# Performance work log

Hardware: AMD Instinct MI355X
Metric: run time of the kernel (lower is better)

Reference implementation:

```python
import jax, jax.numpy as jnp
import numpy as np

N, E, G = 20000, 480000, 200
HID = 32  # hidden_channels


def setup_inputs() -> dict:
    key = jax.random.key(0)
    ks = jax.random.split(key, 40)
    rn = lambda k, shape, s=0.1: jax.random.normal(k, shape, jnp.float32) * s
    inp = {
        "x": jax.random.normal(ks[0], (N, 8), jnp.float32),
        "edge_index": jax.random.randint(ks[1], (2, E), 0, N),
        "edge_attr": jax.random.normal(ks[2], (E, 4), jnp.float32),
        "batch": jnp.sort(jax.random.randint(ks[3], (N,), 0, G)),
        "descriptors": jax.random.normal(ks[4], (G, 48), jnp.float32),
        # edge encoder Linear(4 -> 32)
        "We_enc": rn(ks[5], (4, HID)), "be_enc": rn(ks[6], (HID,)),
        # gat1: GATConv(8 -> 32, heads=4, concat)
        "W1": rn(ks[7], (8, 4 * HID)), "as1": rn(ks[8], (4, HID)), "ad1": rn(ks[9], (4, HID)), "b1": rn(ks[10], (4 * HID,)),
        # gat2: GATConv(128 -> 32, heads=4, concat, edge_dim=32)
        "W2": rn(ks[11], (4 * HID, 4 * HID)), "We2": rn(ks[12], (HID, 4 * HID)),
        "as2": rn(ks[13], (4, HID)), "ad2": rn(ks[14], (4, HID)), "ae2": rn(ks[15], (4, HID)), "b2": rn(ks[16], (4 * HID,)),
        # gat3
        "W3": rn(ks[17], (4 * HID, 4 * HID)), "We3": rn(ks[18], (HID, 4 * HID)),
        "as3": rn(ks[19], (4, HID)), "ad3": rn(ks[20], (4, HID)), "ae3": rn(ks[21], (4, HID)), "b3": rn(ks[22], (4 * HID,)),
        # gat4: heads=1, concat=False
        "W4": rn(ks[23], (4 * HID, HID)), "We4": rn(ks[24], (HID, HID)),
        "as4": rn(ks[25], (1, HID)), "ad4": rn(ks[26], (1, HID)), "ae4": rn(ks[27], (1, HID)), "b4": rn(ks[28], (HID,)),
        # descriptor net Linear(48 -> 32)
        "Wd": rn(ks[29], (48, HID)), "bd": rn(ks[30], (HID,)),
        # final Linear(64 -> 1)
        "Wl": rn(ks[31], (2 * HID, 1)), "bl": rn(ks[32], (1,)),
    }
    return inp


def _gat(x, src, dst, n, W, att_s, att_d, bias, heads, ch, concat, e=None, We=None, att_e=None):
    """PyG GATConv: add self-loops (edge fill='mean'), edge softmax over incoming edges."""
    loops = jnp.arange(n)
    if e is not None:
        cnt = jnp.zeros((n,), x.dtype).at[dst].add(1.0)
        loop_e = jnp.zeros((n, e.shape[1]), x.dtype).at[dst].add(e) / jnp.maximum(cnt, 1.0)[:, None]
        e = jnp.concatenate([e, loop_e], axis=0)  # [E+N, edge_dim]
    s = jnp.concatenate([src, loops])
    d = jnp.concatenate([dst, loops])
    h = (x @ W).reshape(n, heads, ch)                      # [N,H,C]
    a_s = (h * att_s).sum(-1)                              # [N,H]
    a_d = (h * att_d).sum(-1)
    alpha = a_s[s] + a_d[d]                                # [E+N,H]
    if e is not None:
        eh = (e @ We).reshape(-1, heads, ch)
        alpha = alpha + (eh * att_e).sum(-1)
    alpha = jax.nn.leaky_relu(alpha, 0.2)
    amax = jax.ops.segment_max(alpha, d, num_segments=n)
    ex = jnp.exp(alpha - amax[d])
    den = jax.ops.segment_sum(ex, d, num_segments=n)
    alpha = ex / (den[d] + 1e-16)
    out = jax.ops.segment_sum(alpha[:, :, None] * h[s], d, num_segments=n)  # [N,H,C]
    out = out.reshape(n, heads * ch) if concat else out.mean(axis=1)
    return out + bias


def reference(x, edge_index, edge_attr, batch, descriptors,
              We_enc, be_enc,
              W1, as1, ad1, b1,
              W2, We2, as2, ad2, ae2, b2,
              W3, We3, as3, ad3, ae3, b3,
              W4, We4, as4, ad4, ae4, b4,
              Wd, bd, Wl, bl):
    src, dst = edge_index[0], edge_index[1]
    n = x.shape[0]
    edge_emb = edge_attr @ We_enc + be_enc                # [E,32]
    h = jax.nn.relu(_gat(x, src, dst, n, W1, as1, ad1, b1, 4, HID, True))
    h = jax.nn.relu(_gat(h, src, dst, n, W2, as2, ad2, b2, 4, HID, True, edge_emb, We2, ae2))
    h = jax.nn.relu(_gat(h, src, dst, n, W3, as3, ad3, b3, 4, HID, True, edge_emb, We3, ae3))
    h = _gat(h, src, dst, n, W4, as4, ad4, b4, 1, HID, False, edge_emb, We4, ae4)  # [N,32]
    # global mean pool per graph
    g_sum = jax.ops.segment_sum(h, batch, num_segments=G)
    g_cnt = jax.ops.segment_sum(jnp.ones((n,), h.dtype), batch, num_segments=G)
    graph_emb = g_sum / jnp.maximum(g_cnt, 1.0)[:, None]  # [G,32]
    desc_emb = jax.nn.relu(descriptors @ Wd + bd)          # [G,32]
    combined = jnp.concatenate([graph_emb, desc_emb], axis=1)
    return jax.nn.sigmoid(combined @ Wl + bl).reshape(-1)  # [G]
```

## Files before the change

kernel.cpp:

```cpp
#include <hip/hip_runtime.h>
#include <hip/hip_bf16.h>
#include <math.h>

#define NN 20000
#define EE 480000
#define GG 200
#define CAP 96

typedef unsigned int uint32;

static __device__ inline unsigned short f2bf(float f) {
  __hip_bfloat16 h = __float2bfloat16(f);
  return *reinterpret_cast<const unsigned short*>(&h);
}
static __device__ inline float bf2f(unsigned short u) {
  return __uint_as_float(((uint32)u) << 16);
}
static __device__ inline float bf_lo(uint32 u) { return __uint_as_float(u << 16); }
static __device__ inline float bf_hi(uint32 u) { return __uint_as_float(u & 0xffff0000u); }
static __device__ inline uint32 pack2(float lo, float hi) {
  return ((uint32)f2bf(lo)) | (((uint32)f2bf(hi)) << 16);
}

__global__ void hist_kernel(const int* __restrict__ dst, int* __restrict__ cnt) {
  int i = blockIdx.x * 256 + threadIdx.x;
  if (i < EE) atomicAdd(&cnt[dst[i]], 1);
}

__global__ void scan1_kernel(const int* __restrict__ cnt, int* __restrict__ row_ptr,
                             int* __restrict__ partial) {
  __shared__ int buf[1024];
  int t = threadIdx.x;
  int i = blockIdx.x * 1024 + t;
  int v = (i < NN) ? cnt[i] : 0;
  buf[t] = v;
  __syncthreads();
  for (int offd = 1; offd < 1024; offd <<= 1) {
    int tmp = (t >= offd) ? buf[t - offd] : 0;
    __syncthreads();
    buf[t] += tmp;
    __syncthreads();
  }
  if (i < NN) row_ptr[i + 1] = buf[t];
  if (t == 1023) partial[blockIdx.x] = buf[1023];
}

__global__ void scan2_kernel(int* __restrict__ partial, int nblk) {
  int t = threadIdx.x;
  int v = (t < nblk) ? partial[t] : 0;
  for (int offd = 1; offd < 32; offd <<= 1) {
    int u = __shfl_up(v, offd);
    if (t >= offd) v += u;
  }
  if (t < nblk) partial[t] = v;
}

__global__ void scan3_kernel(int* __restrict__ row_ptr, const int* __restrict__ partial) {
  int i = blockIdx.x * 256 + threadIdx.x;
  if (i == 0) row_ptr[0] = 0;
  if (i >= 1 && i <= NN) {
    int b = (i - 1) >> 10;
    if (b > 0) row_ptr[i] += partial[b - 1];
  }
}

__global__ void scatter_kernel(const int* __restrict__ src, const int* __restrict__ dst,
                               const float* __restrict__ attr, const int* __restrict__ row_ptr,
                               int* __restrict__ pos, int* __restrict__ csr_src,
                               uint2* __restrict__ attr_pk) {
  int e = blockIdx.x * 256 + threadIdx.x;
  if (e >= EE) return;
  int d = dst[e];
  int p = row_ptr[d] + atomicAdd(&pos[d], 1);
  csr_src[p] = src[e];
  float4 a = ((const float4*)attr)[e];
  uint2 q;
  q.x = pack2(a.x, a.y);
  q.y = pack2(a.z, a.w);
  attr_pk[p] = q;
}

#define AMB ((NN + 255) / 256)

__global__ void aux_kernel(const int* __restrict__ row_ptr, const uint2* __restrict__ attr_pk,
                           float* __restrict__ mean_attr, const int* __restrict__ batch,
                           int* __restrict__ bound, const float* __restrict__ We_enc,
                           const float* __restrict__ be_enc, const float* __restrict__ We2,
                           const float* __restrict__ ae2, const float* __restrict__ We3,
                           const float* __restrict__ ae3, const float* __restrict__ We4,
                           const float* __restrict__ ae4, float* __restrict__ fold) {
  int b = blockIdx.x;
  int t = threadIdx.x;
  if (b < AMB) {
    int node = b * 256 + t;
    if (node < NN) {
      int p0 = row_ptr[node], p1 = row_ptr[node + 1];
      float s0 = 0.f, s1 = 0.f, s2 = 0.f, s3 = 0.f;
      for (int p = p0; p < p1; ++p) {
        uint2 q = attr_pk[p];
        s0 += bf_lo(q.x); s1 += bf_hi(q.x);
        s2 += bf_lo(q.y); s3 += bf_hi(q.y);
      }
      int deg = p1 - p0;
      float inv = 1.f / (float)(deg > 1 ? deg : 1);
      ((float4*)mean_attr)[node] = make_float4(s0 * inv, s1 * inv, s2 * inv, s3 * inv);
    }
    return;
  }
  if (b < 2 * AMB) {
    int i = (b - AMB) * 256 + t;
    if (i >= NN) return;
    int bc = batch[i];
    int bp = (i == 0) ? -1 : batch[i - 1];
    for (int g = bp + 1; g <= bc; ++g) bound[g] = i;
    if (i == NN - 1)
      for (int g = bc + 1; g <= GG; ++g) bound[g] = NN;
    return;
  }
  __shared__ float V[32 * 4];
  if (t < 128) {
    int k = t >> 2, h = t & 3;
    float s = 0.f;
    for (int c = 0; c < 32; ++c) s = fmaf(We2[k * 128 + h * 32 + c], ae2[h * 32 + c], s);
    V[k * 4 + h] = s;
  }
  __syncthreads();
  if (t < 16) {
    int i = t >> 2, h = t & 3;
    float s = 0.f;
    for (int k = 0; k < 32; ++k) s = fmaf(We_enc[i * 32 + k], V[k * 4 + h], s);
    fold[i * 4 + h] = s;
  } else if (t < 20) {
    int h = t - 16;
    float s = 0.f;
    for (int k = 0; k < 32; ++k) s = fmaf(be_enc[k], V[k * 4 + h], s);
    fold[16 + h] = s;
  }
  __syncthreads();
  if (t < 128) {
    int k = t >> 2, h = t & 3;
    float s = 0.f;
    for (int c = 0; c < 32; ++c) s = fmaf(We3[k * 128 + h * 32 + c], ae3[h * 32 + c], s);
    V[k * 4 + h] = s;
  }
  __syncthreads();
  if (t < 16) {
    int i = t >> 2, h = t & 3;
    float s = 0.f;
    for (int k = 0; k < 32; ++k) s = fmaf(We_enc[i * 32 + k], V[k * 4 + h], s);
    fold[20 + i * 4 + h] = s;
  } else if (t < 20) {
    int h = t - 16;
    float s = 0.f;
    for (int k = 0; k < 32; ++k) s = fmaf(be_enc[k], V[k * 4 + h], s);
    fold[36 + h] = s;
  }
  __syncthreads();
  if (t < 32) {
    float s = 0.f;
    for (int c = 0; c < 32; ++c) s = fmaf(We4[t * 32 + c], ae4[c], s);
    V[t] = s;
  }
  __syncthreads();
  if (t < 4) {
    float s = 0.f;
    for (int k = 0; k < 32; ++k) s = fmaf(We_enc[t * 32 + k], V[k], s);
    fold[40 + t] = s;
  } else if (t == 4) {
    float s = 0.f;
    for (int k = 0; k < 32; ++k) s = fmaf(be_enc[k], V[k], s);
    fold[44] = s;
  }
}

__global__ void gemm1_kernel(const float* __restrict__ X, const float* __restrict__ W,
                             const float* __restrict__ att_s, const float* __restrict__ att_d,
                             __hip_bfloat16* __restrict__ H, float* __restrict__ a_s,
                             float* __restrict__ a_d) {
  constexpr int K = 8;
  constexpr int COLS = 128;
  constexpr int ROWS = 8;
  __shared__ float xs[ROWS][K];
  int tid = threadIdx.x;
  int row0 = blockIdx.x * ROWS;
  if (tid < ROWS * K) xs[tid / K][tid % K] = X[row0 * K + tid];
  __syncthreads();
  int c = tid;
  float acc[ROWS];
#pragma unroll
  for (int j = 0; j < ROWS; ++j) acc[j] = 0.f;
  for (int k = 0; k < K; ++k) {
    float wv = W[k * COLS + c];
#pragma unroll
    for (int j = 0; j < ROWS; ++j) acc[j] = fmaf(xs[j][k], wv, acc[j]);
  }
  float asv = att_s[c], adv = att_d[c];
#pragma unroll
  for (int j = 0; j < ROWS; ++j) {
    int row = row0 + j;
    float vs = acc[j] * asv, vd = acc[j] * adv;
#pragma unroll
    for (int m = 16; m >= 1; m >>= 1) {
      vs += __shfl_xor(vs, m);
      vd += __shfl_xor(vd, m);
    }
    H[row * COLS + c] = __float2bfloat16(acc[j]);
    if ((tid & 31) == 0) {
      a_s[row * 4 + (c >> 5)] = vs;
      a_d[row * 4 + (c >> 5)] = vd;
    }
  }
}

template <int COLS, int TR>
__global__ __launch_bounds__(256) void gemm2_kernel(const float* __restrict__ X,
                                                    const float* __restrict__ W,
                                                    const float* __restrict__ att_s,
                                                    const float* __restrict__ att_d,
                                                    __hip_bfloat16* __restrict__ H,
                                                    float* __restrict__ a_s,
                                                    float* __restrict__ a_d) {
  constexpr int K = 128;
  constexpr int HEADS = COLS / 32;
  constexpr int CG = COLS / 4;
  constexpr int RG = 256 / CG;
  constexpr int ROWS = RG * TR;
  __shared__ unsigned short ws[K * COLS];
  __shared__ float xs[ROWS * K];
  int tid = threadIdx.x;
  int row0 = blockIdx.x * ROWS;
  for (int i = tid * 4; i < K * COLS; i += 1024) {
    float4 wv = *(const float4*)&W[i];
    ushort4 u;
    u.x = f2bf(wv.x); u.y = f2bf(wv.y); u.z = f2bf(wv.z); u.w = f2bf(wv.w);
    *(ushort4*)&ws[i] = u;
  }
  for (int i = tid * 4; i < ROWS * K; i += 1024) {
    int grow = row0 + i / K;
    float4 v = make_float4(0.f, 0.f, 0.f, 0.f);
    if (grow < NN) v = *(const float4*)&X[(size_t)grow * K + (i & (K - 1))];
    *(float4*)&xs[i] = v;
  }
  __syncthreads();
  int cg = tid % CG, rg = tid / CG;
  int c0 = cg * 4, r0 = rg * TR;
  float acc[TR][4];
#pragma unroll
  for (int i = 0; i < TR; ++i)
#pragma unroll
    for (int j = 0; j < 4; ++j) acc[i][j] = 0.f;
  for (int k0 = 0; k0 < K; k0 += 4) {
    float w4[4][4];
#pragma unroll
    for (int j = 0; j < 4; ++j) {
      ushort4 u = *(ushort4*)&ws[(k0 + j) * COLS + c0];
      w4[j][0] = bf2f(u.x); w4[j][1] = bf2f(u.y); w4[j][2] = bf2f(u.z); w4[j][3] = bf2f(u.w);
    }
#pragma unroll
    for (int i = 0; i < TR; ++i) {
      float4 xv = *(float4*)&xs[(r0 + i) * K + k0];
#pragma unroll
      for (int j = 0; j < 4; ++j) {
        acc[i][j] = fmaf(xv.x, w4[0][j], acc[i][j]);
        acc[i][j] = fmaf(xv.y, w4[1][j], acc[i][j]);
        acc[i][j] = fmaf(xv.z, w4[2][j], acc[i][j]);
        acc[i][j] = fmaf(xv.w, w4[3][j], acc[i][j]);
      }
    }
  }
  float as4[4], ad4[4];
#pragma unroll
  for (int j = 0; j < 4; ++j) { as4[j] = att_s[c0 + j]; ad4[j] = att_d[c0 + j]; }
  int h = c0 >> 5;
#pragma unroll
  for (int i = 0; i < TR; ++i) {
    int row = row0 + r0 + i;
    ushort4 hv;
    hv.x = f2bf(acc[i][0]); hv.y = f2bf(acc[i][1]); hv.z = f2bf(acc[i][2]); hv.w = f2bf(acc[i][3]);
    if (row < NN) *(ushort4*)&H[(size_t)row * COLS + c0] = hv;
    float vs = 0.f, vd = 0.f;
#pragma unroll
    for (int j = 0; j < 4; ++j) {
      vs = fmaf(acc[i][j], as4[j], vs);
      vd = fmaf(acc[i][j], ad4[j], vd);
    }
#pragma unroll
    for (int m = 1; m <= 4; m <<= 1) {
      vs += __shfl_xor(vs, m);
      vd += __shfl_xor(vd, m);
    }
    if ((tid & 7) == 0 && row < NN) {
      a_s[row * HEADS + h] = vs;
      a_d[row * HEADS + h] = vd;
    }
  }
}

template <int HEADS, bool RELU, bool HAS_EDGE>
__global__ __launch_bounds__(256) void gat_agg4_kernel(
    const __hip_bfloat16* __restrict__ Hh, const float* __restrict__ a_s,
    const float* __restrict__ a_d, const uint2* __restrict__ attr_pk,
    const float* __restrict__ mean_attr, const float* __restrict__ foldM,
    const float* __restrict__ foldC, const int* __restrict__ row_ptr,
    const int* __restrict__ csr_src, const float* __restrict__ bias,
    float* __restrict__ out) {
  constexpr int COLS = HEADS * 32;
  constexpr int NL = COLS / 2;
  constexpr int NPB = 256 / NL;
  constexpr int EPP = 16;
  constexpr int JMAX = CAP / EPP;

  int tid = threadIdx.x;
  int ln = tid % NL;
  int node = blockIdx.x * NPB + tid / NL;
  int p0 = row_ptr[node], p1 = row_ptr[node + 1];
  int deg = p1 - p0;
  int base = (tid & 63) & ~(NL - 1);
  const uint32* H32 = (const uint32*)Hh;
  int c = 2 * ln;
  int hc = (HEADS == 4) ? (c >> 5) : 0;

  if (deg > CAP) {
    float gm0 = 0.f, gm1 = 0.f, gm2 = 0.f, gm3 = 0.f, gc = 0.f;
    if (HAS_EDGE) {
      if (HEADS == 4) {
        gm0 = foldM[hc]; gm1 = foldM[4 + hc]; gm2 = foldM[8 + hc]; gm3 = foldM[12 + hc];
        gc = foldC[hc];
      } else {
        gm0 = foldM[0]; gm1 = foldM[1]; gm2 = foldM[2]; gm3 = foldM[3];
        gc = foldC[0];
      }
    }
    float adv = a_d[node * HEADS + hc];
    float al = a_s[node * HEADS + hc] + adv;
    if (HAS_EDGE) {
      float4 m4 = ((const float4*)mean_attr)[node];
      al += fmaf(m4.x, gm0, fmaf(m4.y, gm1, fmaf(m4.z, gm2, fmaf(m4.w, gm3, gc))));
    }
    al = al >= 0.f ? al : 0.2f * al;
    float m = al;
    for (int p = p0; p < p1; ++p) {
      int s = csr_src[p];
      float a = a_s[s * HEADS + hc] + adv;
      if (HAS_EDGE) {
        uint2 q = attr_pk[p];
        a += fmaf(bf_lo(q.x), gm0,
                  fmaf(bf_hi(q.x), gm1, fmaf(bf_lo(q.y), gm2, fmaf(bf_hi(q.y), gm3, gc))));
      }
      a = a >= 0.f ? a : 0.2f * a;
      m = fmaxf(m, a);
    }
    float e0 = __expf(al - m);
    float den = e0;
    uint32 u0 = H32[(size_t)node * NL + ln];
    float acc0 = e0 * bf_lo(u0), acc1 = e0 * bf_hi(u0);
    for (int p = p0; p < p1; ++p) {
      int s = csr_src[p];
      float a = a_s[s * HEADS + hc] + adv;
      if (HAS_EDGE) {
        uint2 q = attr_pk[p];
        a += fmaf(bf_lo(q.x), gm0,
                  fmaf(bf_hi(q.x), gm1, fmaf(bf_lo(q.y), gm2, fmaf(bf_hi(q.y), gm3, gc))));
      }
      a = a >= 0.f ? a : 0.2f * a;
      float ex = __expf(a - m);
      den += ex;
      uint32 u = H32[(size_t)s * NL + ln];
      acc0 = fmaf(ex, bf_lo(u), acc0);
      acc1 = fmaf(ex, bf_hi(u), acc1);
    }
    float inv = 1.f / (den + 1e-16f);
    float o0 = acc0 * inv + bias[c];
    float o1 = acc1 * inv + bias[c + 1];
    if (RELU) { o0 = fmaxf(o0, 0.f); o1 = fmaxf(o1, 0.f); }
    *(float2*)&out[(size_t)node * COLS + c] = make_float2(o0, o1);
    return;
  }

  int p_rel = ln / HEADS;
  int h = ln % HEADS;
  float adv = a_d[node * HEADS + h];
  float fm0 = 0.f, fm1 = 0.f, fm2 = 0.f, fm3 = 0.f, fc = 0.f;
  if (HAS_EDGE) {
    if (HEADS == 4) {
      fm0 = foldM[h]; fm1 = foldM[4 + h]; fm2 = foldM[8 + h]; fm3 = foldM[12 + h];
      fc = foldC[h];
    } else {
      fm0 = foldM[0]; fm1 = foldM[1]; fm2 = foldM[2]; fm3 = foldM[3];
      fc = foldC[0];
    }
  }

  float av[JMAX];
  int sv[JMAX];
  float mpart = -1e30f;
#pragma unroll
  for (int j = 0; j < JMAX; ++j) {
    int pr = p_rel + j * EPP;
    av[j] = -1e30f;
    sv[j] = 0;
    if (pr < deg) {
      int p = p0 + pr;
      int s = csr_src[p];
      sv[j] = s;
      float a = a_s[s * HEADS + h] + adv;
      if (HAS_EDGE) {
        uint2 q = attr_pk[p];
        a += fmaf(bf_lo(q.x), fm0,
                  fmaf(bf_hi(q.x), fm1, fmaf(bf_lo(q.y), fm2, fmaf(bf_hi(q.y), fm3, fc))));
      }
      a = a >= 0.f ? a : 0.2f * a;
      av[j] = a;
      mpart = fmaxf(mpart, a);
    }
  }
  float al = -1e30f;
  if (p_rel == 0) {
    al = a_s[node * HEADS + h] + adv;
    if (HAS_EDGE && deg > 0) {
      float4 m4 = ((const float4*)mean_attr)[node];
      al += fmaf(m4.x, fm0, fmaf(m4.y, fm1, fmaf(m4.z, fm2, fmaf(m4.w, fm3, fc))));
    }
    al = al >= 0.f ? al : 0.2f * al;
    mpart = fmaxf(mpart, al);
  }
  float mfull = mpart;
#pragma unroll
  for (int m = HEADS; m < NL; m <<= 1) mfull = fmaxf(mfull, __shfl_xor(mfull, m));

  float dpart = 0.f;
#pragma unroll
  for (int j = 0; j < JMAX; ++j) {
    av[j] = __expf(av[j] - mfull);
    dpart += av[j];
  }
  float exl = 0.f;
  if (p_rel == 0) {
    exl = __expf(al - mfull);
    dpart += exl;
  }
  float den = dpart;
#pragma unroll
  for (int m = HEADS; m < NL; m <<= 1) den += __shfl_xor(den, m);

  float exl_c = __shfl(exl, base + hc);
  float den_c = __shfl(den, base + hc);
  uint32 u0 = H32[(size_t)node * NL + ln];
  float acc0 = exl_c * bf_lo(u0);
  float acc1 = exl_c * bf_hi(u0);
#pragma unroll
  for (int j = 0; j < JMAX; ++j) {
    if (j * EPP < deg) {
      float exv[EPP];
      int sval[EPP];
#pragma unroll
      for (int pp = 0; pp < EPP; ++pp) {
        int srcl = base + pp * HEADS + hc;
        exv[pp] = __shfl(av[j], srcl);
        sval[pp] = __shfl(sv[j], srcl);
      }
      uint32 uv[EPP];
#pragma unroll
      for (int pp = 0; pp < EPP; ++pp) uv[pp] = H32[(size_t)sval[pp] * NL + ln];
#pragma unroll
      for (int pp = 0; pp < EPP; ++pp) {
        acc0 = fmaf(exv[pp], bf_lo(uv[pp]), acc0);
        acc1 = fmaf(exv[pp], bf_hi(uv[pp]), acc1);
      }
    }
  }
  float inv = 1.f / (den_c + 1e-16f);
  float o0 = acc0 * inv + bias[c];
  float o1 = acc1 * inv + bias[c + 1];
  if (RELU) { o0 = fmaxf(o0, 0.f); o1 = fmaxf(o1, 0.f); }
  *(float2*)&out[(size_t)node * COLS + c] = make_float2(o0, o1);
}

__global__ void pool_final_kernel(const float* __restrict__ h4, const int* __restrict__ bound,
                                  const float* __restrict__ desc, const float* __restrict__ Wd,
                                  const float* __restrict__ bd, const float* __restrict__ Wl,
                                  const float* __restrict__ bl, float* __restrict__ outp) {
  __shared__ float part[8][32];
  int g = blockIdx.x;
  int tid = threadIdx.x;
  int r0 = bound[g], r1 = bound[g + 1];
  int cch = tid & 31, chunk = tid >> 5;
  float s = 0.f;
  for (int r = r0 + chunk; r < r1; r += 8) s += h4[r * 32 + cch];
  part[chunk][cch] = s;
  __syncthreads();
  if (tid < 64) {
    float v;
    if (tid < 32) {
      float tot = 0.f;
#pragma unroll
      for (int k = 0; k < 8; ++k) tot += part[k][tid];
      int rows = r1 - r0;
      float cnt = (float)(rows > 1 ? rows : 1);
      v = (tot / cnt) * Wl[tid];
    } else {
      int cc = tid - 32;
      float acc = bd[cc];
      for (int k = 0; k < 48; ++k) acc = fmaf(desc[g * 48 + k], Wd[k * 32 + cc], acc);
      v = fmaxf(acc, 0.f) * Wl[32 + cc];
    }
#pragma unroll
    for (int m = 32; m >= 1; m >>= 1) v += __shfl_xor(v, m);
    if (tid == 0) outp[g] = 1.f / (1.f + expf(-(v + bl[0])));
  }
}

extern "C" void kernel_launch(void* const* d_in, const int* in_sizes, int n_in,
                              void* d_out, int out_size, void* d_ws, size_t ws_size,
                              hipStream_t stream) {
  const float* x = (const float*)d_in[0];
  const int* ei = (const int*)d_in[1];
  const float* edge_attr = (const float*)d_in[2];
  const int* batch = (const int*)d_in[3];
  const float* desc = (const float*)d_in[4];
  const float* We_enc = (const float*)d_in[5];
  const float* be_enc = (const float*)d_in[6];
  const float* W1 = (const float*)d_in[7];
  const float* as1 = (const float*)d_in[8];
  const float* ad1 = (const float*)d_in[9];
  const float* b1 = (const float*)d_in[10];
  const float* W2 = (const float*)d_in[11];
  const float* We2 = (const float*)d_in[12];
  const float* as2 = (const float*)d_in[13];
  const float* ad2 = (const float*)d_in[14];
  const float* ae2 = (const float*)d_in[15];
  const float* b2 = (const float*)d_in[16];
  const float* W3 = (const float*)d_in[17];
  const float* We3 = (const float*)d_in[18];
  const float* as3 = (const float*)d_in[19];
  const float* ad3 = (const float*)d_in[20];
  const float* ae3 = (const float*)d_in[21];
  const float* b3 = (const float*)d_in[22];
  const float* W4 = (const float*)d_in[23];
  const float* We4 = (const float*)d_in[24];
  const float* as4 = (const float*)d_in[25];
  const float* ad4 = (const float*)d_in[26];
  const float* ae4 = (const float*)d_in[27];
  const float* b4 = (const float*)d_in[28];
  const float* Wd = (const float*)d_in[29];
  const float* bd = (const float*)d_in[30];
  const float* Wl = (const float*)d_in[31];
  const float* bl = (const float*)d_in[32];

  const int* srcp = ei;
  const int* dstp = ei + EE;

  char* w = (char*)d_ws;
  size_t off = 0;
  auto take = [&](size_t nbytes) -> void* {
    void* p = (void*)(w + off);
    off += (nbytes + 255) & ~(size_t)255;
    return p;
  };
  int* cnt = (int*)take(2 * NN * 4);
  int* pos = cnt + NN;
  int* row_ptr = (int*)take((NN + 1) * 4);
  int* csr_src = (int*)take((size_t)EE * 4);
  uint2* attr_pk = (uint2*)take((size_t)EE * 8);
  float* mean_attr = (float*)take(NN * 16);
  float* fold = (float*)take(48 * 4);
  int* partial = (int*)take(64 * 4);
  int* bound = (int*)take((GG + 1) * 4);
  float* a_s = (float*)take(NN * 16);
  float* a_d = (float*)take(NN * 16);
  __hip_bfloat16* hbuf = (__hip_bfloat16*)take((size_t)NN * 128 * 2);
  float* obuf = (float*)take((size_t)NN * 128 * 4);
  (void)ws_size;

  constexpr int NSCAN = (NN + 1023) / 1024;

  hipMemsetAsync(cnt, 0, 2 * NN * 4, stream);
  hist_kernel<<<(EE + 255) / 256, 256, 0, stream>>>(dstp, cnt);
  scan1_kernel<<<NSCAN, 1024, 0, stream>>>(cnt, row_ptr, partial);
  scan2_kernel<<<1, 64, 0, stream>>>(partial, NSCAN);
  scan3_kernel<<<(NN + 256) / 256, 256, 0, stream>>>(row_ptr, partial);
  scatter_kernel<<<(EE + 255) / 256, 256, 0, stream>>>(srcp, dstp, edge_attr, row_ptr, pos,
                                                       csr_src, attr_pk);
  aux_kernel<<<2 * AMB + 1, 256, 0, stream>>>(row_ptr, attr_pk, mean_attr, batch, bound, We_enc,
                                              be_enc, We2, ae2, We3, ae3, We4, ae4, fold);

  gemm1_kernel<<<NN / 8, 128, 0, stream>>>(x, W1, as1, ad1, hbuf, a_s, a_d);
  gat_agg4_kernel<4, true, false><<<NN / 4, 256, 0, stream>>>(
      hbuf, a_s, a_d, nullptr, nullptr, nullptr, nullptr, row_ptr, csr_src, b1, obuf);
  gemm2_kernel<128, 4><<<NN / 32, 256, 0, stream>>>(obuf, W2, as2, ad2, hbuf, a_s, a_d);
  gat_agg4_kernel<4, true, true><<<NN / 4, 256, 0, stream>>>(
      hbuf, a_s, a_d, attr_pk, mean_attr, fold + 0, fold + 16, row_ptr, csr_src, b2, obuf);
  gemm2_kernel<128, 4><<<NN / 32, 256, 0, stream>>>(obuf, W3, as3, ad3, hbuf, a_s, a_d);
  gat_agg4_kernel<4, true, true><<<NN / 4, 256, 0, stream>>>(
      hbuf, a_s, a_d, attr_pk, mean_attr, fold + 20, fold + 36, row_ptr, csr_src, b3, obuf);
  gemm2_kernel<32, 2><<<(NN + 63) / 64, 256, 0, stream>>>(obuf, W4, as4, ad4, hbuf, a_s, a_d);
  gat_agg4_kernel<1, false, true><<<NN / 16, 256, 0, stream>>>(
      hbuf, a_s, a_d, attr_pk, mean_attr, fold + 40, fold + 44, row_ptr, csr_src, b4, obuf);

  pool_final_kernel<<<GG, 256, 0, stream>>>(obuf, bound, desc, Wd, bd, Wl, bl, (float*)d_out);
}
```

Measured before the change: 341.6 us.

## Fuse histogram with gemm1, merge scan kernels, stage softmax weights in LDS

Merges the edge-degree histogram and the first-layer projection into one launch using disjoint block ranges, and folds the scan2/scan3 steps into a single kernel. This removes two kernel launches and lets independent work run concurrently. In the aggregation kernel, exponentiated attention weights and source indices are written to shared memory and read back per edge instead of being broadcast through lane shuffles. This trades shuffle instructions for LDS traffic and adds shared-memory usage, which may lower occupancy.

```diff
diff --git a/kernel.cpp b/kernel.cpp
--- a/kernel.cpp
+++ b/kernel.cpp
@@ -22,10 +22,53 @@
   return ((uint32)f2bf(lo)) | (((uint32)f2bf(hi)) << 16);
 }
 
-__global__ void hist_kernel(const int* __restrict__ dst, int* __restrict__ cnt) {
-  int i = blockIdx.x * 256 + threadIdx.x;
-  if (i < EE) atomicAdd(&cnt[dst[i]], 1);
-}
+#define HB ((EE + 255) / 256)
+#define GB (NN / 16)
+
+__global__ void histgemm1_kernel(const int* __restrict__ dst, int* __restrict__ cnt,
+                                 const float* __restrict__ X, const float* __restrict__ W,
+                                 const float* __restrict__ att_s, const float* __restrict__ att_d,
+                                 __hip_bfloat16* __restrict__ H, float* __restrict__ a_s,
+                                 float* __restrict__ a_d) {
+  int tid = threadIdx.x;
+  if (blockIdx.x < HB) {
+    int i = blockIdx.x * 256 + tid;
+    if (i < EE) atomicAdd(&cnt[dst[i]], 1);
+    return;
+  }
+  __shared__ float xs[16][8];
+  int row0 = (blockIdx.x - HB) * 16;
+  if (tid < 128) xs[tid >> 3][tid & 7] = X[row0 * 8 + tid];
+  __syncthreads();
+  int c = tid & 127;
+  int half = tid >> 7;
+  float acc[8];
+#pragma unroll
+  for (int j = 0; j < 8; ++j) acc[j] = 0.f;
+  for (int k = 0; k < 8; ++k) {
+    float wv = W[k * 128 + c];
+#pragma unroll
+    for (int j = 0; j < 8; ++j) acc[j] = fmaf(xs[half * 8 + j][k], wv, acc[j]);
+  }
+  float asv = att_s[c], adv = att_d[c];
+#pragma unroll
+  for (int j = 0; j < 8; ++j) {
+    int row = row0 + half * 8 + j;
+    float vs = acc[j] * asv, vd = acc[j] * adv;
+#pragma unroll
+    for (int m = 16; m >= 1; m >>= 1) {
+      vs += __shfl_xor(vs, m);
+      vd += __shfl_xor(vd, m);
+    }
+    H[row * 128 + c] = __float2bfloat16(acc[j]);
+    if ((tid & 31) == 0) {
+      a_s[row * 4 + (c >> 5)] = vs;
+      a_d[row * 4 + (c >> 5)] = vd;
+    }
+  }
+}
+
+#define NSCAN ((NN + 1023) / 1024)
 
 __global__ void scan1_kernel(const int* __restrict__ cnt, int* __restrict__ row_ptr,
                              int* __restrict__ partial) {
@@ -45,22 +88,23 @@
   if (t == 1023) partial[blockIdx.x] = buf[1023];
 }
 
-__global__ void scan2_kernel(int* __restrict__ partial, int nblk) {
+__global__ void scan23_kernel(int* __restrict__ row_ptr, const int* __restrict__ partial) {
+  __shared__ int sc[NSCAN];
   int t = threadIdx.x;
-  int v = (t < nblk) ? partial[t] : 0;
-  for (int offd = 1; offd < 32; offd <<= 1) {
-    int u = __shfl_up(v, offd);
-    if (t >= offd) v += u;
-  }
-  if (t < nblk) partial[t] = v;
-}
-
-__global__ void scan3_kernel(int* __restrict__ row_ptr, const int* __restrict__ partial) {
-  int i = blockIdx.x * 256 + threadIdx.x;
+  if (t < 64) {
+    int v = (t < NSCAN) ? partial[t] : 0;
+    for (int o = 1; o < 32; o <<= 1) {
+      int u = __shfl_up(v, o);
+      if (t >= o) v += u;
+    }
+    if (t < NSCAN) sc[t] = v;
+  }
+  __syncthreads();
+  int i = blockIdx.x * 256 + t;
   if (i == 0) row_ptr[0] = 0;
   if (i >= 1 && i <= NN) {
     int b = (i - 1) >> 10;
-    if (b > 0) row_ptr[i] += partial[b - 1];
+    if (b > 0) row_ptr[i] += sc[b - 1];
   }
 }
 
@@ -170,45 +214,6 @@
     float s = 0.f;
     for (int k = 0; k < 32; ++k) s = fmaf(be_enc[k], V[k], s);
     fold[44] = s;
-  }
-}
-
-__global__ void gemm1_kernel(const float* __restrict__ X, const float* __restrict__ W,
-                             const float* __restrict__ att_s, const float* __restrict__ att_d,
-                             __hip_bfloat16* __restrict__ H, float* __restrict__ a_s,
-                             float* __restrict__ a_d) {
-  constexpr int K = 8;
-  constexpr int COLS = 128;
-  constexpr int ROWS = 8;
-  __shared__ float xs[ROWS][K];
-  int tid = threadIdx.x;
-  int row0 = blockIdx.x * ROWS;
-  if (tid < ROWS * K) xs[tid / K][tid % K] = X[row0 * K + tid];
-  __syncthreads();
-  int c = tid;
-  float acc[ROWS];
-#pragma unroll
-  for (int j = 0; j < ROWS; ++j) acc[j] = 0.f;
-  for (int k = 0; k < K; ++k) {
-    float wv = W[k * COLS + c];
-#pragma unroll
-    for (int j = 0; j < ROWS; ++j) acc[j] = fmaf(xs[j][k], wv, acc[j]);
-  }
-  float asv = att_s[c], adv = att_d[c];
-#pragma unroll
-  for (int j = 0; j < ROWS; ++j) {
-    int row = row0 + j;
-    float vs = acc[j] * asv, vd = acc[j] * adv;
-#pragma unroll
-    for (int m = 16; m >= 1; m >>= 1) {
-      vs += __shfl_xor(vs, m);
-      vd += __shfl_xor(vd, m);
-    }
-    H[row * COLS + c] = __float2bfloat16(acc[j]);
-    if ((tid & 31) == 0) {
-      a_s[row * 4 + (c >> 5)] = vs;
-      a_d[row * 4 + (c >> 5)] = vd;
-    }
   }
 }
 
@@ -297,7 +302,7 @@
 }
 
 template <int HEADS, bool RELU, bool HAS_EDGE>
-__global__ __launch_bounds__(256) void gat_agg4_kernel(
+__global__ __launch_bounds__(256) void gat_agg5_kernel(
     const __hip_bfloat16* __restrict__ Hh, const float* __restrict__ a_s,
     const float* __restrict__ a_d, const uint2* __restrict__ attr_pk,
     const float* __restrict__ mean_attr, const float* __restrict__ foldM,
@@ -309,10 +314,16 @@
   constexpr int NPB = 256 / NL;
   constexpr int EPP = 16;
   constexpr int JMAX = CAP / EPP;
+  constexpr int EXS = CAP * HEADS + (HEADS == 1 ? 1 : 0);
+  constexpr int SRS = CAP + (HEADS == 1 ? 1 : 0);
+
+  __shared__ float ex_lds[NPB][EXS];
+  __shared__ int src_lds[NPB][SRS];
 
   int tid = threadIdx.x;
   int ln = tid % NL;
-  int node = blockIdx.x * NPB + tid / NL;
+  int nl = tid / NL;
+  int node = blockIdx.x * NPB + nl;
   int p0 = row_ptr[node], p1 = row_ptr[node + 1];
   int deg = p1 - p0;
   int base = (tid & 63) & ~(NL - 1);
@@ -392,17 +403,15 @@
   }
 
   float av[JMAX];
-  int sv[JMAX];
   float mpart = -1e30f;
 #pragma unroll
   for (int j = 0; j < JMAX; ++j) {
     int pr = p_rel + j * EPP;
     av[j] = -1e30f;
-    sv[j] = 0;
+    int s = 0;
     if (pr < deg) {
       int p = p0 + pr;
-      int s = csr_src[p];
-      sv[j] = s;
+      s = csr_src[p];
       float a = a_s[s * HEADS + h] + adv;
       if (HAS_EDGE) {
         uint2 q = attr_pk[p];
@@ -413,6 +422,7 @@
       av[j] = a;
       mpart = fmaxf(mpart, a);
     }
+    if (HEADS == 1 || h == 0) src_lds[nl][pr] = s;
   }
   float al = -1e30f;
   if (p_rel == 0) {
@@ -431,8 +441,10 @@
   float dpart = 0.f;
 #pragma unroll
   for (int j = 0; j < JMAX; ++j) {
-    av[j] = __expf(av[j] - mfull);
-    dpart += av[j];
+    int pr = p_rel + j * EPP;
+    float ex = __expf(av[j] - mfull);
+    ex_lds[nl][pr * HEADS + h] = ex;
+    dpart += ex;
   }
   float exl = 0.f;
   if (p_rel == 0) {
@@ -455,9 +467,9 @@
       int sval[EPP];
 #pragma unroll
       for (int pp = 0; pp < EPP; ++pp) {
-        int srcl = base + pp * HEADS + hc;
-        exv[pp] = __shfl(av[j], srcl);
-        sval[pp] = __shfl(sv[j], srcl);
+        int p = j * EPP + pp;
+        sval[pp] = src_lds[nl][p];
+        exv[pp] = ex_lds[nl][p * HEADS + hc];
       }
       uint32 uv[EPP];
 #pragma unroll
@@ -572,29 +584,25 @@
   float* obuf = (float*)take((size_t)NN * 128 * 4);
   (void)ws_size;
 
-  constexpr int NSCAN = (NN + 1023) / 1024;
-
   hipMemsetAsync(cnt, 0, 2 * NN * 4, stream);
-  hist_kernel<<<(EE + 255) / 256, 256, 0, stream>>>(dstp, cnt);
+  histgemm1_kernel<<<HB + GB, 256, 0, stream>>>(dstp, cnt, x, W1, as1, ad1, hbuf, a_s, a_d);
   scan1_kernel<<<NSCAN, 1024, 0, stream>>>(cnt, row_ptr, partial);
-  scan2_kernel<<<1, 64, 0, stream>>>(partial, NSCAN);
-  scan3_kernel<<<(NN + 256) / 256, 256, 0, stream>>>(row_ptr, partial);
+  scan23_kernel<<<(NN + 256) / 256, 256, 0, stream>>>(row_ptr, partial);
   scatter_kernel<<<(EE + 255) / 256, 256, 0, stream>>>(srcp, dstp, edge_attr, row_ptr, pos,
                                                        csr_src, attr_pk);
   aux_kernel<<<2 * AMB + 1, 256, 0, stream>>>(row_ptr, attr_pk, mean_attr, batch, bound, We_enc,
                                               be_enc, We2, ae2, We3, ae3, We4, ae4, fold);
 
-  gemm1_kernel<<<NN / 8, 128, 0, stream>>>(x, W1, as1, ad1, hbuf, a_s, a_d);
-  gat_agg4_kernel<4, true, false><<<NN / 4, 256, 0, stream>>>(
+  gat_agg5_kernel<4, true, false><<<NN / 4, 256, 0, stream>>>(
       hbuf, a_s, a_d, nullptr, nullptr, nullptr, nullptr, row_ptr, csr_src, b1, obuf);
   gemm2_kernel<128, 4><<<NN / 32, 256, 0, stream>>>(obuf, W2, as2, ad2, hbuf, a_s, a_d);
-  gat_agg4_kernel<4, true, true><<<NN / 4, 256, 0, stream>>>(
+  gat_agg5_kernel<4, true, true><<<NN / 4, 256, 0, stream>>>(
       hbuf, a_s, a_d, attr_pk, mean_attr, fold + 0, fold + 16, row_ptr, csr_src, b2, obuf);
   gemm2_kernel<128, 4><<<NN / 32, 256, 0, stream>>>(obuf, W3, as3, ad3, hbuf, a_s, a_d);
-  gat_agg4_kernel<4, true, true><<<NN / 4, 256, 0, stream>>>(
+  gat_agg5_kernel<4, true, true><<<NN / 4, 256, 0, stream>>>(
       hbuf, a_s, a_d, attr_pk, mean_attr, fold + 20, fold + 36, row_ptr, csr_src, b3, obuf);
   gemm2_kernel<32, 2><<<(NN + 63) / 64, 256, 0, stream>>>(obuf, W4, as4, ad4, hbuf, a_s, a_d);
-  gat_agg4_kernel<1, false, true><<<NN / 16, 256, 0, stream>>>(
+  gat_agg5_kernel<1, false, true><<<NN / 16, 256, 0, stream>>>(
       hbuf, a_s, a_d, attr_pk, mean_attr, fold + 40, fold + 44, row_ptr, csr_src, b4, obuf);
 
   pool_final_kernel<<<GG, 256, 0, stream>>>(obuf, bound, desc, Wd, bd, Wl, bl, (float*)d_out);
```

Measured after the change: 331.8 us. 2.9% less time.
